# Kernel optimization log

Measured on AMD Instinct MI355X. Metric: run time of the kernel, lower is better.

The kernel has to match this reference:

```python
import jax, jax.numpy as jnp
import numpy as np

N_NODES = 100000
N_EDGES = 3200000
D_IN = 256
D_OUT = 256


def setup_inputs() -> dict:
    key = jax.random.key(0)
    k1, k2, k3, k4, k5 = jax.random.split(key, 5)
    x = jax.random.normal(k1, (N_NODES, D_IN), dtype=jnp.float32)
    edge_row = jax.random.randint(k2, (N_EDGES,), 0, N_NODES, dtype=jnp.int32)
    edge_col = jax.random.randint(k3, (N_EDGES,), 0, N_NODES, dtype=jnp.int32)
    edge_val = jax.random.uniform(k4, (N_EDGES,), dtype=jnp.float32)
    # Linear weight [out_dim, in_dim], kaiming-uniform-like scale
    bound = 1.0 / np.sqrt(D_IN)
    W = jax.random.uniform(k5, (D_OUT, D_IN), dtype=jnp.float32,
                           minval=-bound, maxval=bound)
    return {"x": x, "edge_row": edge_row, "edge_col": edge_col,
            "edge_val": edge_val, "W": W}


def reference(x, edge_row, edge_col, edge_val, W):
    # SpMM: agg[i] = sum_{edges e with row=i} val_e * x[col_e]
    msgs = edge_val[:, None] * x[edge_col]            # [E, D_IN] gather
    agg = jax.ops.segment_sum(msgs, edge_row, num_segments=N_NODES)  # [N, D_IN]
    # Dense linear projection (bias=False): agg @ W.T
    return agg @ W.T                                  # [N, D_OUT]
```

## Files before the change

kernel.cpp:

```cpp
#include <hip/hip_runtime.h>
#include <hip/hip_bf16.h>
#include <stdint.h>

#define N_NODES 100000
#define N_EDGES 3200000
#define D_FEAT 256
#define NBKT 391
#define CHUNK 8192
#define NBLK_E 391

typedef __attribute__((ext_vector_type(8))) short short8;
typedef __attribute__((ext_vector_type(8))) ushort ushort8;
typedef __attribute__((ext_vector_type(4))) float float4v;

__device__ inline unsigned short f2bf(float f) {
    union { float f; unsigned u; } v; v.f = f;
    unsigned u = v.u;
    u += 0x7FFF + ((u >> 16) & 1);
    return (unsigned short)(u >> 16);
}
__device__ inline float bf2f(unsigned short u) {
    union { unsigned u; float f; } v; v.u = (unsigned)u << 16;
    return v.f;
}

__global__ __launch_bounds__(256) void xconv_kernel(const float4* __restrict__ x4,
                                                    ushort4* __restrict__ xbf4) {
    int i = blockIdx.x * 256 + threadIdx.x;
    float4 v = x4[i];
    ushort4 o;
    o.x = f2bf(v.x); o.y = f2bf(v.y); o.z = f2bf(v.z); o.w = f2bf(v.w);
    xbf4[i] = o;
}


__global__ __launch_bounds__(256) void coarse_hist(const int* __restrict__ erow,
                                                   int* __restrict__ hist) {
    __shared__ int cnt[NBKT];
    for (int b = threadIdx.x; b < NBKT; b += 256) cnt[b] = 0;
    __syncthreads();
    int cb = blockIdx.x * CHUNK;
    for (int j = 0; j < CHUNK; j += 256) {
        int i = cb + j + threadIdx.x;
        if (i < N_EDGES) atomicAdd(&cnt[erow[i] >> 8], 1);
    }
    __syncthreads();
    for (int b = threadIdx.x; b < NBKT; b += 256)
        hist[blockIdx.x * NBKT + b] = cnt[b];
}

__global__ __launch_bounds__(512) void scan_blocks(int* __restrict__ hist,
                                                   int* __restrict__ totals) {
    __shared__ int s[512];
    int b = blockIdx.x;
    int t = threadIdx.x;
    int v = (t < NBLK_E) ? hist[t * NBKT + b] : 0;
    s[t] = v;
    __syncthreads();
    for (int o = 1; o < 512; o <<= 1) {
        int x = (t >= o) ? s[t - o] : 0;
        __syncthreads();
        s[t] += x;
        __syncthreads();
    }
    if (t < NBLK_E) hist[t * NBKT + b] = s[t] - v;
    if (t == NBLK_E - 1) totals[b] = s[t];
}

__global__ __launch_bounds__(512) void scan_buckets(const int* __restrict__ totals,
                                                    int* __restrict__ base_,
                                                    int* __restrict__ row_start) {
    __shared__ int s[512];
    int t = threadIdx.x;
    int v = (t < NBKT) ? totals[t] : 0;
    s[t] = v;
    __syncthreads();
    for (int o = 1; o < 512; o <<= 1) {
        int x = (t >= o) ? s[t - o] : 0;
        __syncthreads();
        s[t] += x;
        __syncthreads();
    }
    if (t < NBKT) base_[t] = s[t] - v;
    if (t == 0) { base_[NBKT] = N_EDGES; row_start[N_NODES] = N_EDGES; }
}

__global__ __launch_bounds__(256) void coarse_scatter(
        const int* __restrict__ erow, const int* __restrict__ ecol,
        const float* __restrict__ eval,
        const int* __restrict__ hist, const int* __restrict__ base_,
        uint2* __restrict__ tmp) {
    __shared__ int lbase[NBKT];
    __shared__ int cnt[NBKT];
    for (int b = threadIdx.x; b < NBKT; b += 256) {
        lbase[b] = hist[blockIdx.x * NBKT + b] + base_[b];
        cnt[b] = 0;
    }
    __syncthreads();
    int cb = blockIdx.x * CHUNK;
    for (int j = 0; j < CHUNK; j += 256) {
        int i = cb + j + threadIdx.x;
        if (i < N_EDGES) {
            int r = erow[i];
            int b = r >> 8;
            int pos = lbase[b] + atomicAdd(&cnt[b], 1);
            uint2 cv;
            cv.x = (unsigned)ecol[i] | ((unsigned)(r & 255) << 17);
            union { float f; unsigned u; } w; w.f = eval[i];
            cv.y = w.u;
            tmp[pos] = cv;
        }
    }
}

__global__ __launch_bounds__(256) void fine_sort(const uint2* __restrict__ tmp,
                                                 const int* __restrict__ base_,
                                                 uint2* __restrict__ csr,
                                                 int* __restrict__ row_start) {
    __shared__ int cnt[256];
    __shared__ int excl[256];
    int b = blockIdx.x;
    int t = threadIdx.x;
    int s0 = base_[b];
    int nb = base_[b + 1] - s0;
    cnt[t] = 0;
    __syncthreads();
    for (int j = t; j < nb; j += 256)
        atomicAdd(&cnt[tmp[s0 + j].x >> 17], 1);
    __syncthreads();
    int v = cnt[t];
    excl[t] = v;
    __syncthreads();
    for (int o = 1; o < 256; o <<= 1) {
        int x = (t >= o) ? excl[t - o] : 0;
        __syncthreads();
        excl[t] += x;
        __syncthreads();
    }
    int ex = excl[t] - v;
    int row = b * 256 + t;
    if (row < N_NODES) row_start[row] = s0 + ex;
    excl[t] = ex;
    cnt[t] = 0;
    __syncthreads();
    for (int j = t; j < nb; j += 256) {
        uint2 cv = tmp[s0 + j];
        unsigned rl = cv.x >> 17;
        int dst = s0 + excl[rl] + atomicAdd(&cnt[rl], 1);
        csr[dst] = cv;
    }
}

__global__ __launch_bounds__(256) void spmm_kernel(
        const ushort* __restrict__ xbf,
        const int* __restrict__ row_start,
        const uint2* __restrict__ csr_cv,
        ushort* __restrict__ agg_bf) {
    int row  = (blockIdx.x * blockDim.x + threadIdx.x) >> 6;
    int lane = threadIdx.x & 63;
    int half = lane >> 5;
    int hl   = lane & 31;
    if (row >= N_NODES) return;
    int start = row_start[row];
    int end   = row_start[row + 1];
    float acc[8] = {0.f, 0.f, 0.f, 0.f, 0.f, 0.f, 0.f, 0.f};
    int e = start + half;
    for (; e + 2 < end; e += 4) {
        uint2 cv0 = csr_cv[e];
        uint2 cv1 = csr_cv[e + 2];
        ushort8 v0 = *(const ushort8*)&xbf[(size_t)(cv0.x & 0x1FFFF) * 256 + hl * 8];
        ushort8 v1 = *(const ushort8*)&xbf[(size_t)(cv1.x & 0x1FFFF) * 256 + hl * 8];
        union { unsigned u; float f; } w0, w1;
        w0.u = cv0.y; w1.u = cv1.y;
        #pragma unroll
        for (int j = 0; j < 8; ++j) acc[j] += w0.f * bf2f(v0[j]);
        #pragma unroll
        for (int j = 0; j < 8; ++j) acc[j] += w1.f * bf2f(v1[j]);
    }
    for (; e < end; e += 2) {
        uint2 cv = csr_cv[e];
        ushort8 v = *(const ushort8*)&xbf[(size_t)(cv.x & 0x1FFFF) * 256 + hl * 8];
        union { unsigned u; float f; } w; w.u = cv.y;
        #pragma unroll
        for (int j = 0; j < 8; ++j) acc[j] += w.f * bf2f(v[j]);
    }
    #pragma unroll
    for (int j = 0; j < 8; ++j) acc[j] += __shfl_xor(acc[j], 32, 64);
    if (half == 0) {
        ushort8 o;
        #pragma unroll
        for (int j = 0; j < 8; ++j) o[j] = f2bf(acc[j]);
        *(ushort8*)&agg_bf[(size_t)row * 256 + hl * 8] = o;
    }
}

__global__ void wconv_kernel(const float* __restrict__ W, ushort* __restrict__ Wbf) {
    int i = blockIdx.x * 256 + threadIdx.x;
    Wbf[i] = f2bf(W[i]);
}

__global__ __launch_bounds__(256) void gemm_kernel(
        const ushort* __restrict__ Abf,
        const ushort* __restrict__ Wbf,
        float* __restrict__ out) {
    int w    = threadIdx.x >> 6;
    int lane = threadIdx.x & 63;
    int quad = lane >> 4;
    int l16  = lane & 15;
    int rt   = blockIdx.x * 64;

    float4v acc[4][4];
    #pragma unroll
    for (int mt = 0; mt < 4; ++mt)
        #pragma unroll
        for (int nt = 0; nt < 4; ++nt) acc[mt][nt] = (float4v){0.f, 0.f, 0.f, 0.f};

    #pragma unroll
    for (int k0 = 0; k0 < 256; k0 += 32) {
        short8 a[4], bf[4];
        #pragma unroll
        for (int mt = 0; mt < 4; ++mt) {
            int row = rt + mt * 16 + l16;
            if (row >= N_NODES) row = N_NODES - 1;
            a[mt] = *(const short8*)&Abf[(size_t)row * 256 + k0 + quad * 8];
        }
        #pragma unroll
        for (int nt = 0; nt < 4; ++nt) {
            int n = w * 64 + nt * 16 + l16;
            bf[nt] = *(const short8*)&Wbf[n * 256 + k0 + quad * 8];
        }
        #pragma unroll
        for (int mt = 0; mt < 4; ++mt)
            #pragma unroll
            for (int nt = 0; nt < 4; ++nt)
                acc[mt][nt] = __builtin_amdgcn_mfma_f32_16x16x32_bf16(a[mt], bf[nt], acc[mt][nt], 0, 0, 0);
    }
    #pragma unroll
    for (int mt = 0; mt < 4; ++mt)
        #pragma unroll
        for (int nt = 0; nt < 4; ++nt) {
            int n = w * 64 + nt * 16 + l16;
            #pragma unroll
            for (int r = 0; r < 4; ++r) {
                int row = rt + mt * 16 + quad * 4 + r;
                if (row < N_NODES) out[(size_t)row * 256 + n] = acc[mt][nt][r];
            }
        }
}


extern "C" void kernel_launch(void* const* d_in, const int* in_sizes, int n_in,
                              void* d_out, int out_size, void* d_ws, size_t ws_size,
                              hipStream_t stream) {
    const float* x    = (const float*)d_in[0];
    const int*   erow = (const int*)d_in[1];
    const int*   ecol = (const int*)d_in[2];
    const float* eval = (const float*)d_in[3];
    const float* W    = (const float*)d_in[4];
    float* out = (float*)d_out;

    char* ws = (char*)d_ws;
    size_t off = 0;
    int* hist      = (int*)(ws + off);   off += ((size_t)NBLK_E * NBKT * 4 + 255) & ~255ull;
    int* totals    = (int*)(ws + off);   off += ((size_t)NBKT * 4 + 255) & ~255ull;
    int* base_     = (int*)(ws + off);   off += ((size_t)(NBKT + 1) * 4 + 255) & ~255ull;
    int* row_start = (int*)(ws + off);   off += ((size_t)(N_NODES + 1) * 4 + 255) & ~255ull;
    uint2* tmp_cv  = (uint2*)(ws + off); off += (size_t)N_EDGES * 8;
    uint2* csr_cv  = (uint2*)(ws + off); off += (size_t)N_EDGES * 8;
    ushort* Wbf    = (ushort*)(ws + off);  off += (size_t)D_FEAT * D_FEAT * 2;
    ushort* xbf    = (ushort*)(ws + off);  off += (size_t)N_NODES * D_FEAT * 2;
    ushort* agg_bf = (ushort*)(ws + off);  off += (size_t)N_NODES * D_FEAT * 2;

    xconv_kernel<<<(N_NODES * D_FEAT / 4) / 256, 256, 0, stream>>>((const float4*)x, (ushort4*)xbf);
    coarse_hist<<<NBLK_E, 256, 0, stream>>>(erow, hist);
    scan_blocks<<<NBKT, 512, 0, stream>>>(hist, totals);
    scan_buckets<<<1, 512, 0, stream>>>(totals, base_, row_start);
    coarse_scatter<<<NBLK_E, 256, 0, stream>>>(erow, ecol, eval, hist, base_, tmp_cv);
    fine_sort<<<NBKT, 256, 0, stream>>>(tmp_cv, base_, csr_cv, row_start);
    wconv_kernel<<<(D_FEAT * D_FEAT) / 256, 256, 0, stream>>>(W, Wbf);
    spmm_kernel<<<N_NODES / 4, 256, 0, stream>>>(xbf, row_start, csr_cv, agg_bf);
    gemm_kernel<<<(N_NODES + 63) / 64, 256, 0, stream>>>(agg_bf, Wbf, out);
}
```

Before: 593.7 us.

## Reorder to project before aggregation and sort edges by column first

Uses associativity to compute y = x·Wᵀ first in a GEMM that reads fp32 x directly and converts it to bf16 on the fly. The SpMM then gathers rows of y and writes fp32 output directly, which removes the separate x conversion pass and the agg round trip. Edges are first bucketed by column and then stably by row, so gathers within each row follow column order for better cache locality. This adds an extra histogram, scan and scatter pass over the edges plus more workspace, and it unrolls the SpMM loop to four edges per half-wave.

```diff
diff --git a/kernel.cpp b/kernel.cpp
--- a/kernel.cpp
+++ b/kernel.cpp
@@ -1,5 +1,4 @@
 #include <hip/hip_runtime.h>
-#include <hip/hip_bf16.h>
 #include <stdint.h>
 
 #define N_NODES 100000
@@ -24,17 +23,66 @@
     return v.f;
 }
 
-__global__ __launch_bounds__(256) void xconv_kernel(const float4* __restrict__ x4,
-                                                    ushort4* __restrict__ xbf4) {
+__global__ void wconv_kernel(const float* __restrict__ W, ushort* __restrict__ Wbf) {
     int i = blockIdx.x * 256 + threadIdx.x;
-    float4 v = x4[i];
-    ushort4 o;
-    o.x = f2bf(v.x); o.y = f2bf(v.y); o.z = f2bf(v.z); o.w = f2bf(v.w);
-    xbf4[i] = o;
-}
-
-
-__global__ __launch_bounds__(256) void coarse_hist(const int* __restrict__ erow,
+    Wbf[i] = f2bf(W[i]);
+}
+
+__global__ __launch_bounds__(256) void gemm_x_kernel(
+        const float* __restrict__ x,
+        const ushort* __restrict__ Wbf,
+        ushort* __restrict__ ybf) {
+    int w    = threadIdx.x >> 6;
+    int lane = threadIdx.x & 63;
+    int quad = lane >> 4;
+    int l16  = lane & 15;
+    int rt   = blockIdx.x * 64;
+
+    float4v acc[4][4];
+    #pragma unroll
+    for (int mt = 0; mt < 4; ++mt)
+        #pragma unroll
+        for (int nt = 0; nt < 4; ++nt) acc[mt][nt] = (float4v){0.f, 0.f, 0.f, 0.f};
+
+    #pragma unroll
+    for (int k0 = 0; k0 < 256; k0 += 32) {
+        short8 a[4], bf[4];
+        #pragma unroll
+        for (int mt = 0; mt < 4; ++mt) {
+            int row = rt + mt * 16 + l16;
+            if (row >= N_NODES) row = N_NODES - 1;
+            const float4v* p = (const float4v*)&x[(size_t)row * 256 + k0 + quad * 8];
+            float4v f0 = p[0], f1 = p[1];
+            a[mt][0] = (short)f2bf(f0.x); a[mt][1] = (short)f2bf(f0.y);
+            a[mt][2] = (short)f2bf(f0.z); a[mt][3] = (short)f2bf(f0.w);
+            a[mt][4] = (short)f2bf(f1.x); a[mt][5] = (short)f2bf(f1.y);
+            a[mt][6] = (short)f2bf(f1.z); a[mt][7] = (short)f2bf(f1.w);
+        }
+        #pragma unroll
+        for (int nt = 0; nt < 4; ++nt) {
+            int n = w * 64 + nt * 16 + l16;
+            bf[nt] = *(const short8*)&Wbf[n * 256 + k0 + quad * 8];
+        }
+        #pragma unroll
+        for (int mt = 0; mt < 4; ++mt)
+            #pragma unroll
+            for (int nt = 0; nt < 4; ++nt)
+                acc[mt][nt] = __builtin_amdgcn_mfma_f32_16x16x32_bf16(a[mt], bf[nt], acc[mt][nt], 0, 0, 0);
+    }
+    #pragma unroll
+    for (int mt = 0; mt < 4; ++mt)
+        #pragma unroll
+        for (int nt = 0; nt < 4; ++nt) {
+            int n = w * 64 + nt * 16 + l16;
+            #pragma unroll
+            for (int r = 0; r < 4; ++r) {
+                int row = rt + mt * 16 + quad * 4 + r;
+                if (row < N_NODES) ybf[(size_t)row * 256 + n] = f2bf(acc[mt][nt][r]);
+            }
+        }
+}
+
+__global__ __launch_bounds__(256) void coarse_hist(const int* __restrict__ key,
                                                    int* __restrict__ hist) {
     __shared__ int cnt[NBKT];
     for (int b = threadIdx.x; b < NBKT; b += 256) cnt[b] = 0;
@@ -42,7 +90,7 @@
     int cb = blockIdx.x * CHUNK;
     for (int j = 0; j < CHUNK; j += 256) {
         int i = cb + j + threadIdx.x;
-        if (i < N_EDGES) atomicAdd(&cnt[erow[i] >> 8], 1);
+        if (i < N_EDGES) atomicAdd(&cnt[key[i] >> 8], 1);
     }
     __syncthreads();
     for (int b = threadIdx.x; b < NBKT; b += 256)
@@ -85,9 +133,38 @@
     if (t == 0) { base_[NBKT] = N_EDGES; row_start[N_NODES] = N_EDGES; }
 }
 
-__global__ __launch_bounds__(256) void coarse_scatter(
+__global__ __launch_bounds__(256) void col_scatter(
         const int* __restrict__ erow, const int* __restrict__ ecol,
         const float* __restrict__ eval,
+        const int* __restrict__ hist, const int* __restrict__ base_,
+        int* __restrict__ tmpr, uint2* __restrict__ tmpcv) {
+    __shared__ int lbase[NBKT];
+    __shared__ int cnt[NBKT];
+    for (int b = threadIdx.x; b < NBKT; b += 256) {
+        lbase[b] = hist[blockIdx.x * NBKT + b] + base_[b];
+        cnt[b] = 0;
+    }
+    __syncthreads();
+    int cb = blockIdx.x * CHUNK;
+    for (int j = 0; j < CHUNK; j += 256) {
+        int i = cb + j + threadIdx.x;
+        if (i < N_EDGES) {
+            int c = ecol[i];
+            int r = erow[i];
+            int b = c >> 8;
+            int pos = lbase[b] + atomicAdd(&cnt[b], 1);
+            tmpr[pos] = r;
+            uint2 cv;
+            cv.x = (unsigned)c | ((unsigned)(r & 255) << 17);
+            union { float f; unsigned u; } w; w.f = eval[i];
+            cv.y = w.u;
+            tmpcv[pos] = cv;
+        }
+    }
+}
+
+__global__ __launch_bounds__(256) void row_scatter(
+        const int* __restrict__ tmpr, const uint2* __restrict__ tmpcv,
         const int* __restrict__ hist, const int* __restrict__ base_,
         uint2* __restrict__ tmp) {
     __shared__ int lbase[NBKT];
@@ -101,14 +178,9 @@
     for (int j = 0; j < CHUNK; j += 256) {
         int i = cb + j + threadIdx.x;
         if (i < N_EDGES) {
-            int r = erow[i];
-            int b = r >> 8;
+            int b = tmpr[i] >> 8;
             int pos = lbase[b] + atomicAdd(&cnt[b], 1);
-            uint2 cv;
-            cv.x = (unsigned)ecol[i] | ((unsigned)(r & 255) << 17);
-            union { float f; unsigned u; } w; w.f = eval[i];
-            cv.y = w.u;
-            tmp[pos] = cv;
+            tmp[pos] = tmpcv[i];
         }
     }
 }
@@ -152,10 +224,10 @@
 }
 
 __global__ __launch_bounds__(256) void spmm_kernel(
-        const ushort* __restrict__ xbf,
+        const ushort* __restrict__ ybf,
         const int* __restrict__ row_start,
         const uint2* __restrict__ csr_cv,
-        ushort* __restrict__ agg_bf) {
+        float* __restrict__ out) {
     int row  = (blockIdx.x * blockDim.x + threadIdx.x) >> 6;
     int lane = threadIdx.x & 63;
     int half = lane >> 5;
@@ -165,21 +237,29 @@
     int end   = row_start[row + 1];
     float acc[8] = {0.f, 0.f, 0.f, 0.f, 0.f, 0.f, 0.f, 0.f};
     int e = start + half;
-    for (; e + 2 < end; e += 4) {
+    for (; e + 6 < end; e += 8) {
         uint2 cv0 = csr_cv[e];
         uint2 cv1 = csr_cv[e + 2];
-        ushort8 v0 = *(const ushort8*)&xbf[(size_t)(cv0.x & 0x1FFFF) * 256 + hl * 8];
-        ushort8 v1 = *(const ushort8*)&xbf[(size_t)(cv1.x & 0x1FFFF) * 256 + hl * 8];
-        union { unsigned u; float f; } w0, w1;
-        w0.u = cv0.y; w1.u = cv1.y;
+        uint2 cv2 = csr_cv[e + 4];
+        uint2 cv3 = csr_cv[e + 6];
+        ushort8 v0 = *(const ushort8*)&ybf[(size_t)(cv0.x & 0x1FFFF) * 256 + hl * 8];
+        ushort8 v1 = *(const ushort8*)&ybf[(size_t)(cv1.x & 0x1FFFF) * 256 + hl * 8];
+        ushort8 v2 = *(const ushort8*)&ybf[(size_t)(cv2.x & 0x1FFFF) * 256 + hl * 8];
+        ushort8 v3 = *(const ushort8*)&ybf[(size_t)(cv3.x & 0x1FFFF) * 256 + hl * 8];
+        union { unsigned u; float f; } w0, w1, w2, w3;
+        w0.u = cv0.y; w1.u = cv1.y; w2.u = cv2.y; w3.u = cv3.y;
         #pragma unroll
         for (int j = 0; j < 8; ++j) acc[j] += w0.f * bf2f(v0[j]);
         #pragma unroll
         for (int j = 0; j < 8; ++j) acc[j] += w1.f * bf2f(v1[j]);
+        #pragma unroll
+        for (int j = 0; j < 8; ++j) acc[j] += w2.f * bf2f(v2[j]);
+        #pragma unroll
+        for (int j = 0; j < 8; ++j) acc[j] += w3.f * bf2f(v3[j]);
     }
     for (; e < end; e += 2) {
         uint2 cv = csr_cv[e];
-        ushort8 v = *(const ushort8*)&xbf[(size_t)(cv.x & 0x1FFFF) * 256 + hl * 8];
+        ushort8 v = *(const ushort8*)&ybf[(size_t)(cv.x & 0x1FFFF) * 256 + hl * 8];
         union { unsigned u; float f; } w; w.u = cv.y;
         #pragma unroll
         for (int j = 0; j < 8; ++j) acc[j] += w.f * bf2f(v[j]);
@@ -187,65 +267,11 @@
     #pragma unroll
     for (int j = 0; j < 8; ++j) acc[j] += __shfl_xor(acc[j], 32, 64);
     if (half == 0) {
-        ushort8 o;
-        #pragma unroll
-        for (int j = 0; j < 8; ++j) o[j] = f2bf(acc[j]);
-        *(ushort8*)&agg_bf[(size_t)row * 256 + hl * 8] = o;
-    }
-}
-
-__global__ void wconv_kernel(const float* __restrict__ W, ushort* __restrict__ Wbf) {
-    int i = blockIdx.x * 256 + threadIdx.x;
-    Wbf[i] = f2bf(W[i]);
-}
-
-__global__ __launch_bounds__(256) void gemm_kernel(
-        const ushort* __restrict__ Abf,
-        const ushort* __restrict__ Wbf,
-        float* __restrict__ out) {
-    int w    = threadIdx.x >> 6;
-    int lane = threadIdx.x & 63;
-    int quad = lane >> 4;
-    int l16  = lane & 15;
-    int rt   = blockIdx.x * 64;
-
-    float4v acc[4][4];
-    #pragma unroll
-    for (int mt = 0; mt < 4; ++mt)
-        #pragma unroll
-        for (int nt = 0; nt < 4; ++nt) acc[mt][nt] = (float4v){0.f, 0.f, 0.f, 0.f};
-
-    #pragma unroll
-    for (int k0 = 0; k0 < 256; k0 += 32) {
-        short8 a[4], bf[4];
-        #pragma unroll
-        for (int mt = 0; mt < 4; ++mt) {
-            int row = rt + mt * 16 + l16;
-            if (row >= N_NODES) row = N_NODES - 1;
-            a[mt] = *(const short8*)&Abf[(size_t)row * 256 + k0 + quad * 8];
-        }
-        #pragma unroll
-        for (int nt = 0; nt < 4; ++nt) {
-            int n = w * 64 + nt * 16 + l16;
-            bf[nt] = *(const short8*)&Wbf[n * 256 + k0 + quad * 8];
-        }
-        #pragma unroll
-        for (int mt = 0; mt < 4; ++mt)
-            #pragma unroll
-            for (int nt = 0; nt < 4; ++nt)
-                acc[mt][nt] = __builtin_amdgcn_mfma_f32_16x16x32_bf16(a[mt], bf[nt], acc[mt][nt], 0, 0, 0);
-    }
-    #pragma unroll
-    for (int mt = 0; mt < 4; ++mt)
-        #pragma unroll
-        for (int nt = 0; nt < 4; ++nt) {
-            int n = w * 64 + nt * 16 + l16;
-            #pragma unroll
-            for (int r = 0; r < 4; ++r) {
-                int row = rt + mt * 16 + quad * 4 + r;
-                if (row < N_NODES) out[(size_t)row * 256 + n] = acc[mt][nt][r];
-            }
-        }
+        float4v o0 = {acc[0], acc[1], acc[2], acc[3]};
+        float4v o1 = {acc[4], acc[5], acc[6], acc[7]};
+        *(float4v*)&out[(size_t)row * 256 + hl * 8]     = o0;
+        *(float4v*)&out[(size_t)row * 256 + hl * 8 + 4] = o1;
+    }
 }
 
 
@@ -265,19 +291,25 @@
     int* totals    = (int*)(ws + off);   off += ((size_t)NBKT * 4 + 255) & ~255ull;
     int* base_     = (int*)(ws + off);   off += ((size_t)(NBKT + 1) * 4 + 255) & ~255ull;
     int* row_start = (int*)(ws + off);   off += ((size_t)(N_NODES + 1) * 4 + 255) & ~255ull;
+    int* tmpr      = (int*)(ws + off);   off += ((size_t)N_EDGES * 4 + 255) & ~255ull;
+    uint2* tmpcv   = (uint2*)(ws + off); off += (size_t)N_EDGES * 8;
     uint2* tmp_cv  = (uint2*)(ws + off); off += (size_t)N_EDGES * 8;
     uint2* csr_cv  = (uint2*)(ws + off); off += (size_t)N_EDGES * 8;
     ushort* Wbf    = (ushort*)(ws + off);  off += (size_t)D_FEAT * D_FEAT * 2;
-    ushort* xbf    = (ushort*)(ws + off);  off += (size_t)N_NODES * D_FEAT * 2;
-    ushort* agg_bf = (ushort*)(ws + off);  off += (size_t)N_NODES * D_FEAT * 2;
-
-    xconv_kernel<<<(N_NODES * D_FEAT / 4) / 256, 256, 0, stream>>>((const float4*)x, (ushort4*)xbf);
-    coarse_hist<<<NBLK_E, 256, 0, stream>>>(erow, hist);
+    ushort* ybf    = (ushort*)(ws + off);  off += (size_t)N_NODES * D_FEAT * 2;
+
+    wconv_kernel<<<(D_FEAT * D_FEAT) / 256, 256, 0, stream>>>(W, Wbf);
+    gemm_x_kernel<<<(N_NODES + 63) / 64, 256, 0, stream>>>(x, Wbf, ybf);
+
+    coarse_hist<<<NBLK_E, 256, 0, stream>>>(ecol, hist);
     scan_blocks<<<NBKT, 512, 0, stream>>>(hist, totals);
     scan_buckets<<<1, 512, 0, stream>>>(totals, base_, row_start);
-    coarse_scatter<<<NBLK_E, 256, 0, stream>>>(erow, ecol, eval, hist, base_, tmp_cv);
+    col_scatter<<<NBLK_E, 256, 0, stream>>>(erow, ecol, eval, hist, base_, tmpr, tmpcv);
+    coarse_hist<<<NBLK_E, 256, 0, stream>>>(tmpr, hist);
+    scan_blocks<<<NBKT, 512, 0, stream>>>(hist, totals);
+    scan_buckets<<<1, 512, 0, stream>>>(totals, base_, row_start);
+    row_scatter<<<NBLK_E, 256, 0, stream>>>(tmpr, tmpcv, hist, base_, tmp_cv);
     fine_sort<<<NBKT, 256, 0, stream>>>(tmp_cv, base_, csr_cv, row_start);
-    wconv_kernel<<<(D_FEAT * D_FEAT) / 256, 256, 0, stream>>>(W, Wbf);
-    spmm_kernel<<<N_NODES / 4, 256, 0, stream>>>(xbf, row_start, csr_cv, agg_bf);
-    gemm_kernel<<<(N_NODES + 63) / 64, 256, 0, stream>>>(agg_bf, Wbf, out);
-}
+
+    spmm_kernel<<<N_NODES / 4, 256, 0, stream>>>(ybf, row_start, csr_cv, out);
+}
```

After: 701.7 us. 18.2% more time.
